# Kernel optimization log

Hardware: AMD Instinct MI355X
Metric: run time of the kernel (lower is better)

## Reference

```python
import jax, jax.numpy as jnp
import numpy as np

N_SAMPLES = 131072
N_FRAMES = 128
CPD = 16
WINDOW = 1024
N_VOICES = 8
N_BLOCKS = 3
N_CP = 512
N_VERBS = 8
MAX_ACTIVE = 32
BASE_RES = 0.5
MAX_GAIN = 5.0
B = 4
E = 16


def fft_convolve(a, b):
    # linear convolution via zero-padded rFFT, truncated to input length
    n = a.shape[-1]
    fa = jnp.fft.rfft(a, n=2 * n, axis=-1)
    fb = jnp.fft.rfft(b, n=2 * n, axis=-1)
    return jnp.fft.irfft(fa * fb, n=2 * n, axis=-1)[..., :n]


def sparsify(x, k):
    # keep top-k entries of the whole control plane, zero the rest
    flat = x.reshape(-1)
    vals, idx = jax.lax.top_k(flat, k)
    return jnp.zeros_like(flat).at[idx].set(vals).reshape(x.shape)


def run_layer(cp, w1, decays, w2, audio_map, gains):
    # cp: [CPD, F]
    frames = cp.shape[-1]
    x = w1 @ cp
    orig = x
    logd = jnp.log(1e-12 + decays)  # [CPD]
    env = jnp.exp(jnp.cumsum(jnp.broadcast_to(logd[:, None], (CPD, frames)), axis=-1))
    x = fft_convolve(x, env)
    x = w2 @ x + orig
    cp_out = jnp.tanh(x * gains[:, None])
    audio = (audio_map @ cp_out).T.reshape(-1)  # [F*WINDOW], frame-major
    return audio, cp_out


def stack_forward(cp, w1s, w2s, audios, decays_p, gains_p, mix):
    wc = cp
    outs = []
    for i in range(N_BLOCKS):
        d = BASE_RES + jax.nn.sigmoid(decays_p[i]) * (1.0 - BASE_RES)
        g = jax.nn.sigmoid(gains_p[i]) * MAX_GAIN
        out, wc = run_layer(jax.nn.relu(wc), w1s[i], d, w2s[i], audios[i], g)
        outs.append(out)
    channels = jnp.stack(outs, axis=0)  # [N_BLOCKS, N_SAMPLES]
    mixed = jnp.einsum('ct,c->t', channels, jax.nn.softmax(mix))
    return mixed / (jnp.max(jnp.abs(mixed)) + 1e-8)  # max_norm


def event_forward(voice_l, cp_choice, amp, room_l, room_mix_l, times,
                  cp_items, verbs, w1, w2, audio_maps, decays, gains, mix):
    vidx = jnp.argmax(voice_l)  # hard voice one-hot (normalize=True -> value 1.0)
    cp = cp_items[jnp.argmax(cp_choice)].reshape(CPD, N_FRAMES)
    cp = sparsify(cp / (cp.sum() + 1e-8), MAX_ACTIVE)
    samples = stack_forward(cp, w1[vidx], w2[vidx], audio_maps[vidx],
                            decays[vidx], gains[vidx], mix[vidx])  # [N_SAMPLES]
    verb = verbs[jnp.argmax(room_l)]  # hard reverb lookup
    wet = fft_convolve(verb, samples)
    vm = jax.nn.softmax(room_mix_l)  # [wet, dry]
    final = wet * vm[0] + samples * vm[1]
    final = final * jnp.abs(amp[0])
    # DiracScheduler: upsample-with-holes then FFT convolve
    step = N_SAMPLES // N_FRAMES
    impulse = jnp.zeros(N_SAMPLES, final.dtype).at[jnp.arange(N_FRAMES) * step].set(times)
    return fft_convolve(final, impulse)


def setup_inputs():
    key = jax.random.key(0)
    ks = jax.random.split(key, 14)
    return {
        'voice': jax.random.normal(ks[0], (B, E, N_VOICES), jnp.float32),
        'control_plane_choice': jax.random.normal(ks[1], (B, E, N_CP), jnp.float32),
        'amplitudes': jax.random.uniform(ks[2], (B, E, 1), jnp.float32),
        'room_choice': jax.random.normal(ks[3], (B, E, N_VERBS), jnp.float32),
        'room_mix': jax.random.normal(ks[4], (B, E, 2), jnp.float32),
        'times': jax.random.uniform(ks[5], (B, E, N_FRAMES), jnp.float32),
        'cp_items': jax.random.uniform(ks[6], (N_CP, N_FRAMES * CPD), jnp.float32),
        'verbs': jax.random.normal(ks[7], (N_VERBS, N_SAMPLES), jnp.float32) * 0.01,
        'w1': jax.random.normal(ks[8], (N_VOICES, N_BLOCKS, CPD, CPD), jnp.float32) * 0.01,
        'w2': jax.random.normal(ks[9], (N_VOICES, N_BLOCKS, CPD, CPD), jnp.float32) * 0.01,
        'audio_maps': jax.random.normal(ks[10], (N_VOICES, N_BLOCKS, WINDOW, CPD), jnp.float32) * 0.01,
        'decays': jax.random.normal(ks[11], (N_VOICES, N_BLOCKS, CPD), jnp.float32),
        'gains': jax.random.normal(ks[12], (N_VOICES, N_BLOCKS, CPD), jnp.float32),
        'mix': jax.random.normal(ks[13], (N_VOICES, N_BLOCKS), jnp.float32),
    }


def reference(voice, control_plane_choice, amplitudes, room_choice, room_mix, times,
              cp_items, verbs, w1, w2, audio_maps, decays, gains, mix):
    per_event = jax.vmap(jax.vmap(event_forward, in_axes=(0,) * 6 + (None,) * 8),
                         in_axes=(0,) * 6 + (None,) * 8)
    return per_event(voice, control_plane_choice, amplitudes, room_choice, room_mix, times,
                     cp_items, verbs, w1, w2, audio_maps, decays, gains, mix)
```

## Files before the change

### kernel.cpp

```cpp
#include <hip/hip_runtime.h>
#include <math.h>

#define NS 131072
#define NFR 128
#define CPDIM 16
#define WIN 1024
#define NVOICE 8
#define NBLK 3
#define NCP 512
#define NVERB 8
#define NEV 64
#define N1 1024
#define NBINS 1025

struct EvParams {
  int vidx, cpidx, ridx;
  float vm0, vm1, amp;
  float mixw0, mixw1, mixw2;
  unsigned int maxslot;
  int pad[6];
};

__global__ void kt_tw(float2* __restrict__ tw) {
  int k = blockIdx.x * 256 + threadIdx.x;
  if (k < 1024) {
    float ang = -3.067961575771282340e-03f * (float)k;
    float s, c;
    sincosf(ang, &s, &c);
    tw[k] = make_float2(c, s);
  }
}

__device__ __forceinline__ void fft1024(float* re, float* im, const float2* twl,
                                        int tid, bool inverse) {
  #pragma unroll
  for (int s = 1; s <= 10; ++s) {
    const int half = 1 << (s - 1);
    const int tsh = 11 - s;
    for (int k = tid; k < 512; k += 256) {
      int j = k & (half - 1);
      int i0 = ((k ^ j) << 1) | j;
      int i1 = i0 + half;
      float2 w = twl[j << tsh];
      float wr = w.x, wi = inverse ? -w.y : w.y;
      float xr = re[i1], xi = im[i1];
      float tr = wr * xr - wi * xi;
      float ti = wr * xi + wi * xr;
      float ur = re[i0], ui = im[i0];
      re[i0] = ur + tr; im[i0] = ui + ti;
      re[i1] = ur - tr; im[i1] = ui - ti;
    }
    __syncthreads();
  }
}

__device__ __forceinline__ void rfft_fwd(const float2* __restrict__ src2, float scale,
                                         float2* __restrict__ dst,
                                         float* re, float* im, float2* twl,
                                         const float2* __restrict__ twg, int tid) {
  for (int i = tid; i < 1024; i += 256) twl[i] = twg[i];
  for (int n = tid; n < 1024; n += 256) {
    int r = __brev(n) >> 22;
    if (n < 512) {
      float2 x = src2[n];
      re[r] = x.x * scale; im[r] = x.y * scale;
    } else { re[r] = 0.0f; im[r] = 0.0f; }
  }
  __syncthreads();
  fft1024(re, im, twl, tid, false);
  for (int k = tid; k <= 1024; k += 256) {
    int km = (1024 - k) & 1023;
    float zr = re[k & 1023], zi = im[k & 1023];
    float mr = re[km], mi = im[km];
    float Are = 0.5f * (zr + mr), Aim = 0.5f * (zi - mi);
    float Bre = 0.5f * (zi + mi), Bim = 0.5f * (mr - zr);
    float wr, wi;
    if (k == 1024) { wr = -1.0f; wi = 0.0f; }
    else { float2 w = twl[k]; wr = w.x; wi = w.y; }
    dst[k] = make_float2(Are + wr * Bre - wi * Bim, Aim + wr * Bim + wi * Bre);
  }
}

__global__ void k0_params(const float* __restrict__ voice, const float* __restrict__ cpc,
                          const float* __restrict__ amps, const float* __restrict__ roomc,
                          const float* __restrict__ roomm, const float* __restrict__ mix,
                          EvParams* __restrict__ P) {
  int e = blockIdx.x;
  int tid = threadIdx.x;
  __shared__ float bvals[64];
  __shared__ int bidx[64];

  if (tid == 0) {
    const float* v = voice + e * NVOICE;
    int vi = 0; float bv = v[0];
    for (int i = 1; i < NVOICE; ++i) if (v[i] > bv) { bv = v[i]; vi = i; }
    P[e].vidx = vi;

    const float* r = roomc + e * NVERB;
    int ri = 0; float br = r[0];
    for (int i = 1; i < NVERB; ++i) if (r[i] > br) { br = r[i]; ri = i; }
    P[e].ridx = ri;

    float m0 = roomm[e * 2 + 0], m1 = roomm[e * 2 + 1];
    float mx = fmaxf(m0, m1);
    float e0 = expf(m0 - mx), e1 = expf(m1 - mx);
    float inv = 1.0f / (e0 + e1);
    P[e].vm0 = e0 * inv;
    P[e].vm1 = e1 * inv;
    P[e].amp = fabsf(amps[e]);

    const float* mm = mix + vi * NBLK;
    float mmx = fmaxf(fmaxf(mm[0], mm[1]), mm[2]);
    float w0 = expf(mm[0] - mmx), w1 = expf(mm[1] - mmx), w2 = expf(mm[2] - mmx);
    float si = 1.0f / (w0 + w1 + w2);
    P[e].mixw0 = w0 * si; P[e].mixw1 = w1 * si; P[e].mixw2 = w2 * si;
    P[e].maxslot = 0u;
  }

  const float* c = cpc + (size_t)e * NCP;
  float bv = -INFINITY; int bi = 0;
  for (int i = tid; i < NCP; i += 64) {
    float x = c[i];
    if (x > bv) { bv = x; bi = i; }
  }
  bvals[tid] = bv; bidx[tid] = bi;
  __syncthreads();
  if (tid == 0) {
    float best = bvals[0]; int besti = bidx[0];
    for (int i = 1; i < 64; ++i) {
      if (bvals[i] > best || (bvals[i] == best && bidx[i] < besti)) { best = bvals[i]; besti = bidx[i]; }
    }
    P[e].cpidx = besti;
  }
}

__global__ __launch_bounds__(256) void kv_fft(const float* __restrict__ verbs,
                                              const float2* __restrict__ twg,
                                              float2* __restrict__ Vhat) {
  __shared__ float re[N1], im[N1];
  __shared__ float2 twl[N1];
  int v = blockIdx.x >> 7, j = blockIdx.x & 127;
  int tid = threadIdx.x;
  rfft_fwd((const float2*)(verbs + (size_t)v * NS + j * WIN), 1.0f,
           Vhat + ((size_t)v * NFR + j) * NBINS, re, im, twl, twg, tid);
}

__global__ __launch_bounds__(256) void k1a_synth(const float* __restrict__ cp_items,
                                                 const float* __restrict__ w1_all,
                                                 const float* __restrict__ w2_all,
                                                 const float* __restrict__ decays,
                                                 const float* __restrict__ gains,
                                                 const EvParams* __restrict__ P,
                                                 float* __restrict__ cp_out_all) {
  __shared__ float cpv[2048];
  __shared__ float wc[2048], xb[2048], yb[2048];
  __shared__ float w1s[256], w2s[256];
  __shared__ float dv[16], gv[16];
  __shared__ float rv[256];
  __shared__ int ri[256];
  __shared__ float s_scale;

  int e = blockIdx.x, tid = threadIdx.x;
  int vidx = P[e].vidx, cpidx = P[e].cpidx;

  float ls = 0.0f;
  for (int i = tid; i < 2048; i += 256) {
    float x = cp_items[(size_t)cpidx * 2048 + i];
    cpv[i] = x;
    ls += x;
  }
  rv[tid] = ls;
  __syncthreads();
  for (int s = 128; s > 0; s >>= 1) { if (tid < s) rv[tid] += rv[tid + s]; __syncthreads(); }
  if (tid == 0) s_scale = 1.0f / (rv[0] + 1e-8f);
  for (int i = tid; i < 2048; i += 256) wc[i] = 0.0f;
  __syncthreads();
  float scale = s_scale;

  for (int it = 0; it < 32; ++it) {
    float bv = -1.0f; int bi = 1 << 30;
    for (int i = tid; i < 2048; i += 256) {
      float x = cpv[i];
      if (x > bv) { bv = x; bi = i; }
    }
    rv[tid] = bv; ri[tid] = bi;
    __syncthreads();
    for (int s = 128; s > 0; s >>= 1) {
      if (tid < s) {
        float ov = rv[tid + s]; int oi = ri[tid + s];
        if (ov > rv[tid] || (ov == rv[tid] && oi < ri[tid])) { rv[tid] = ov; ri[tid] = oi; }
      }
      __syncthreads();
    }
    if (tid == 0) { int mi = ri[0]; wc[mi] = cpv[mi] * scale; cpv[mi] = -2.0f; }
    __syncthreads();
  }

  for (int l = 0; l < NBLK; ++l) {
    int wbase = (vidx * NBLK + l) * 256;
    w1s[tid] = w1_all[wbase + tid];
    w2s[tid] = w2_all[wbase + tid];
    if (tid < 16) {
      float dp = decays[(vidx * NBLK + l) * 16 + tid];
      float sd = 1.0f / (1.0f + expf(-dp));
      dv[tid] = 1e-12f + 0.5f + 0.5f * sd;
      float gp = gains[(vidx * NBLK + l) * 16 + tid];
      gv[tid] = 5.0f / (1.0f + expf(-gp));
    }
    __syncthreads();
    for (int i = tid; i < 2048; i += 256) {
      int cch = i >> 7, f = i & 127;
      float acc = 0.0f;
      #pragma unroll
      for (int k = 0; k < 16; ++k) acc += w1s[cch * 16 + k] * fmaxf(wc[k * 128 + f], 0.0f);
      xb[i] = acc;
    }
    __syncthreads();
    if (tid < 16) {
      float a = 0.0f, d = dv[tid];
      for (int t = 0; t < 128; ++t) { a = d * (a + xb[tid * 128 + t]); yb[tid * 128 + t] = a; }
    }
    __syncthreads();
    for (int i = tid; i < 2048; i += 256) {
      int cch = i >> 7, f = i & 127;
      float acc = xb[i];
      #pragma unroll
      for (int k = 0; k < 16; ++k) acc += w2s[cch * 16 + k] * yb[k * 128 + f];
      float co = tanhf(acc * gv[cch]);
      wc[i] = co;
      cp_out_all[((size_t)e * NBLK + l) * 2048 + i] = co;
    }
    __syncthreads();
  }
}

__global__ __launch_bounds__(256) void k1b_audio(const float* __restrict__ amaps,
                                                 const float* __restrict__ cp_out_all,
                                                 EvParams* __restrict__ P,
                                                 float* __restrict__ mixed) {
  __shared__ float cps[NBLK][16][16];
  __shared__ float red[256];
  int e = blockIdx.x >> 3, fg = blockIdx.x & 7;
  int f0 = fg * 16, tid = threadIdx.x;
  int vidx = P[e].vidx;
  float mw[3] = {P[e].mixw0, P[e].mixw1, P[e].mixw2};

  for (int i = tid; i < NBLK * 256; i += 256) {
    int bl = i >> 8, r = i & 255, cch = r >> 4, fl = r & 15;
    cps[bl][cch][fl] = cp_out_all[((size_t)e * NBLK + bl) * 2048 + cch * 128 + f0 + fl];
  }
  __syncthreads();

  float amax = 0.0f;
  for (int jw = 0; jw < 4; ++jw) {
    int w = jw * 256 + tid;
    float am[NBLK][16];
    #pragma unroll
    for (int bl = 0; bl < NBLK; ++bl) {
      const float* ap = amaps + (((size_t)(vidx * NBLK + bl)) * WIN + w) * CPDIM;
      #pragma unroll
      for (int cch = 0; cch < 16; ++cch) am[bl][cch] = ap[cch] * mw[bl];
    }
    for (int fl = 0; fl < 16; ++fl) {
      float acc = 0.0f;
      #pragma unroll
      for (int bl = 0; bl < NBLK; ++bl)
        #pragma unroll
        for (int cch = 0; cch < 16; ++cch) acc += am[bl][cch] * cps[bl][cch][fl];
      mixed[(size_t)e * NS + (size_t)(f0 + fl) * WIN + w] = acc;
      amax = fmaxf(amax, fabsf(acc));
    }
  }
  red[tid] = amax;
  __syncthreads();
  for (int s = 128; s > 0; s >>= 1) { if (tid < s) red[tid] = fmaxf(red[tid], red[tid + s]); __syncthreads(); }
  if (tid == 0) atomicMax(&P[e].maxslot, __float_as_uint(red[0]));
}

__global__ __launch_bounds__(256) void k2_fwd(const float* __restrict__ mixed,
                                              const EvParams* __restrict__ P,
                                              const float2* __restrict__ twg,
                                              float2* __restrict__ Shat) {
  __shared__ float re[N1], im[N1];
  __shared__ float2 twl[N1];
  int e = blockIdx.x >> 7, p = blockIdx.x & 127;
  int tid = threadIdx.x;
  float invn = 1.0f / (__uint_as_float(P[e].maxslot) + 1e-8f);
  rfft_fwd((const float2*)(mixed + (size_t)e * NS + p * WIN), invn,
           Shat + ((size_t)e * NFR + p) * NBINS, re, im, twl, twg, tid);
}

__global__ __launch_bounds__(256, 4) void k3_conv(const float2* __restrict__ Shat,
                                                  const float2* __restrict__ Vhat,
                                                  const float* __restrict__ times_g,
                                                  const EvParams* __restrict__ P,
                                                  float2* __restrict__ Ohat) {
  __shared__ float Sre[128 * 16], Sim[128 * 16];
  __shared__ float Vre[128 * 16], Vim[128 * 16];
  __shared__ float tms[128];

  int bx = blockIdx.x;
  int e = bx / 65, bg = bx % 65;
  int bin0 = bg * 16;
  int tid = threadIdx.x;
  int b = tid & 15, pg = tid >> 4;
  int p0 = pg * 8;

  int ridx = P[e].ridx;
  float vm0 = P[e].vm0, vm1 = P[e].vm1, amp = P[e].amp;

  const float2* Sg = Shat + (size_t)e * NFR * NBINS;
  const float2* Vg = Vhat + (size_t)ridx * NFR * NBINS;
  for (int i = tid; i < 2048; i += 256) {
    int f = i >> 4, bb = i & 15;
    int bin = bin0 + bb; if (bin > 1024) bin = 1024;
    float2 s = Sg[f * NBINS + bin];
    Sre[i] = s.x; Sim[i] = s.y;
    float2 v = Vg[f * NBINS + bin];
    Vre[i] = v.x; Vim[i] = v.y;
  }
  if (tid < 128) tms[tid] = times_g[e * NFR + tid];
  __syncthreads();

  float ar[8], ai[8];
  #pragma unroll
  for (int t = 0; t < 8; ++t) { ar[t] = 0.0f; ai[t] = 0.0f; }

  for (int ft = 0; ft < pg; ++ft) {
    int f0v = ft * 8;
    float sr[8], si[8];
    #pragma unroll
    for (int ff = 0; ff < 8; ++ff) { int f = f0v + ff; sr[ff] = Sre[f * 16 + b]; si[ff] = Sim[f * 16 + b]; }
    float vr[15], vi[15];
    int jb = p0 - f0v - 7;
    #pragma unroll
    for (int m = 0; m < 15; ++m) { int j = jb + m; vr[m] = Vre[j * 16 + b]; vi[m] = Vim[j * 16 + b]; }
    #pragma unroll
    for (int ff = 0; ff < 8; ++ff) {
      #pragma unroll
      for (int t = 0; t < 8; ++t) {
        int m = 7 - ff + t;
        ar[t] += sr[ff] * vr[m] - si[ff] * vi[m];
        ai[t] += sr[ff] * vi[m] + si[ff] * vr[m];
      }
    }
  }
  {
    float sr[8], si[8];
    #pragma unroll
    for (int ff = 0; ff < 8; ++ff) { int f = p0 + ff; sr[ff] = Sre[f * 16 + b]; si[ff] = Sim[f * 16 + b]; }
    float vr[8], vi[8];
    #pragma unroll
    for (int m = 0; m < 8; ++m) { vr[m] = Vre[m * 16 + b]; vi[m] = Vim[m * 16 + b]; }
    #pragma unroll
    for (int ff = 0; ff < 8; ++ff) {
      #pragma unroll
      for (int t = 0; t < 8; ++t) {
        if (t >= ff) {
          int m = t - ff;
          ar[t] += sr[ff] * vr[m] - si[ff] * vi[m];
          ai[t] += sr[ff] * vi[m] + si[ff] * vr[m];
        }
      }
    }
  }

  __syncthreads();
  #pragma unroll
  for (int t = 0; t < 8; ++t) {
    int p = p0 + t;
    float sre = Sre[p * 16 + b], sim = Sim[p * 16 + b];
    Vre[p * 16 + b] = amp * (vm0 * ar[t] + vm1 * sre);
    Vim[p * 16 + b] = amp * (vm0 * ai[t] + vm1 * sim);
  }
  __syncthreads();

  #pragma unroll
  for (int t = 0; t < 8; ++t) { ar[t] = 0.0f; ai[t] = 0.0f; }

  for (int ft = 0; ft < pg; ++ft) {
    int f0v = ft * 8;
    float trr[8];
    #pragma unroll
    for (int ff = 0; ff < 8; ++ff) trr[ff] = tms[f0v + ff];
    float ur[15], ui[15];
    int jb = p0 - f0v - 7;
    #pragma unroll
    for (int m = 0; m < 15; ++m) { int j = jb + m; ur[m] = Vre[j * 16 + b]; ui[m] = Vim[j * 16 + b]; }
    #pragma unroll
    for (int ff = 0; ff < 8; ++ff) {
      #pragma unroll
      for (int t = 0; t < 8; ++t) {
        int m = 7 - ff + t;
        ar[t] += trr[ff] * ur[m];
        ai[t] += trr[ff] * ui[m];
      }
    }
  }
  {
    float trr[8];
    #pragma unroll
    for (int ff = 0; ff < 8; ++ff) trr[ff] = tms[p0 + ff];
    float ur[8], ui[8];
    #pragma unroll
    for (int m = 0; m < 8; ++m) { ur[m] = Vre[m * 16 + b]; ui[m] = Vim[m * 16 + b]; }
    #pragma unroll
    for (int ff = 0; ff < 8; ++ff) {
      #pragma unroll
      for (int t = 0; t < 8; ++t) {
        if (t >= ff) {
          int m = t - ff;
          ar[t] += trr[ff] * ur[m];
          ai[t] += trr[ff] * ui[m];
        }
      }
    }
  }

  int bin = bin0 + b;
  if (bin <= 1024) {
    float2* Og = Ohat + (size_t)e * NFR * NBINS;
    #pragma unroll
    for (int t = 0; t < 8; ++t) {
      Og[(p0 + t) * NBINS + bin] = make_float2(ar[t], ai[t]);
    }
  }
}

__global__ __launch_bounds__(256) void k4_ifft(const float2* __restrict__ Ohat,
                                               const float2* __restrict__ twg,
                                               float* __restrict__ out,
                                               float* __restrict__ tail) {
  __shared__ float re[N1], im[N1];
  __shared__ float2 twl[N1];
  int e = blockIdx.x >> 7, p = blockIdx.x & 127;
  int tid = threadIdx.x;
  const float2* src = Ohat + ((size_t)e * NFR + p) * NBINS;
  for (int i = tid; i < 1024; i += 256) twl[i] = twg[i];
  __syncthreads();
  for (int k = tid; k < 1024; k += 256) {
    float2 Xk = src[k];
    float2 Xm = src[1024 - k];
    float Are = 0.5f * (Xk.x + Xm.x), Aim = 0.5f * (Xk.y - Xm.y);
    float Dre = 0.5f * (Xk.x - Xm.x), Dim = 0.5f * (Xk.y + Xm.y);
    float2 w = twl[k];
    float Bre = w.x * Dre + w.y * Dim;
    float Bim = w.x * Dim - w.y * Dre;
    int r = __brev(k) >> 22;
    re[r] = Are - Bim;
    im[r] = Aim + Bre;
  }
  __syncthreads();
  fft1024(re, im, twl, tid, true);
  const float inv = 1.0f / (float)N1;
  float2* o2 = (float2*)(out + (size_t)e * NS + (size_t)p * WIN);
  for (int n = tid; n < 512; n += 256) o2[n] = make_float2(re[n] * inv, im[n] * inv);
  float2* t2 = (float2*)(tail + ((size_t)e * NFR + p) * WIN);
  for (int n = tid; n < 512; n += 256) t2[n] = make_float2(re[n + 512] * inv, im[n + 512] * inv);
}

__global__ __launch_bounds__(256) void k5_tail(const float* __restrict__ tail, float* __restrict__ out) {
  size_t idx = (size_t)blockIdx.x * 256 + threadIdx.x;
  if (idx >= (size_t)NEV * 127 * WIN) return;
  int u = (int)(idx & 1023);
  size_t rest = idx >> 10;
  int pm1 = (int)(rest % 127);
  int e = (int)(rest / 127);
  int p = pm1 + 1;
  out[(size_t)e * NS + (size_t)p * WIN + u] += tail[((size_t)e * NFR + pm1) * WIN + u];
}

extern "C" void kernel_launch(void* const* d_in, const int* in_sizes, int n_in,
                              void* d_out, int out_size, void* d_ws, size_t ws_size,
                              hipStream_t stream) {
  (void)in_sizes; (void)n_in; (void)out_size; (void)ws_size;
  const float* voice    = (const float*)d_in[0];
  const float* cpc      = (const float*)d_in[1];
  const float* amps     = (const float*)d_in[2];
  const float* roomc    = (const float*)d_in[3];
  const float* roomm    = (const float*)d_in[4];
  const float* times    = (const float*)d_in[5];
  const float* cp_items = (const float*)d_in[6];
  const float* verbs    = (const float*)d_in[7];
  const float* w1       = (const float*)d_in[8];
  const float* w2       = (const float*)d_in[9];
  const float* amaps    = (const float*)d_in[10];
  const float* decays   = (const float*)d_in[11];
  const float* gains    = (const float*)d_in[12];
  const float* mix      = (const float*)d_in[13];
  float* out = (float*)d_out;

  char* base = (char*)d_ws;
  EvParams* P       = (EvParams*)base;
  float2* twg       = (float2*)(base + 4096);
  float* cp_out_all = (float*)(base + 4096 + 8192);
  float* mixed      = cp_out_all + (size_t)393216;
  float2* Shat      = (float2*)(mixed + (size_t)8388608);
  float2* Vhat      = Shat + (size_t)NEV * NFR * NBINS;
  float* tail  = mixed;
  float2* Ohat = Shat;

  kt_tw<<<4, 256, 0, stream>>>(twg);
  k0_params<<<NEV, 64, 0, stream>>>(voice, cpc, amps, roomc, roomm, mix, P);
  kv_fft<<<NVERB * NFR, 256, 0, stream>>>(verbs, twg, Vhat);
  k1a_synth<<<NEV, 256, 0, stream>>>(cp_items, w1, w2, decays, gains, P, cp_out_all);
  k1b_audio<<<NEV * 8, 256, 0, stream>>>(amaps, cp_out_all, P, mixed);
  k2_fwd<<<NEV * NFR, 256, 0, stream>>>(mixed, P, twg, Shat);
  k3_conv<<<NEV * 65, 256, 0, stream>>>(Shat, Vhat, times, P, Ohat);
  k4_ifft<<<NEV * NFR, 256, 0, stream>>>(Ohat, twg, out, tail);
  k5_tail<<<(NEV * 127 * WIN) / 256, 256, 0, stream>>>(tail, out);
}
```

Baseline: 558.6 us.

## Pad FFT shared arrays, split twiddles, warp-shuffle top-k, atomic overlap-add

Several changes land together. The FFT shared buffers get padding to avoid bank conflicts, and twiddles are split into separate real and imaginary arrays. Spectra use a padded row stride, and k3 stores complex values as float2 with a stride of 17. The top-k sparsify in k1a now keeps values in registers and uses wavefront shuffles instead of shared-memory tree reductions. The separate tail kernel is removed: the output is zeroed first and k4 overlap-adds directly with atomicAdd, which adds an extra full-output zeroing pass and atomic traffic in exchange.

```diff
diff --git a/kernel.cpp b/kernel.cpp
--- a/kernel.cpp
+++ b/kernel.cpp
@@ -12,6 +12,8 @@
 #define NEV 64
 #define N1 1024
 #define NBINS 1025
+#define NBP 1032
+#define IDX(i) ((i) + ((i) >> 5))
 
 struct EvParams {
   int vidx, cpidx, ridx;
@@ -31,7 +33,13 @@
   }
 }
 
-__device__ __forceinline__ void fft1024(float* re, float* im, const float2* twl,
+__global__ __launch_bounds__(256) void kz_zero(float4* __restrict__ out4) {
+  size_t i = (size_t)blockIdx.x * 256 + threadIdx.x;
+  out4[i] = make_float4(0.f, 0.f, 0.f, 0.f);
+}
+
+__device__ __forceinline__ void fft1024(float* re, float* im,
+                                        const float* twr, const float* twi,
                                         int tid, bool inverse) {
   #pragma unroll
   for (int s = 1; s <= 10; ++s) {
@@ -40,9 +48,11 @@
     for (int k = tid; k < 512; k += 256) {
       int j = k & (half - 1);
       int i0 = ((k ^ j) << 1) | j;
-      int i1 = i0 + half;
-      float2 w = twl[j << tsh];
-      float wr = w.x, wi = inverse ? -w.y : w.y;
+      int i1 = IDX(i0 + half);
+      i0 = IDX(i0);
+      float wr = twr[j << tsh];
+      float wi = twi[j << tsh];
+      if (inverse) wi = -wi;
       float xr = re[i1], xi = im[i1];
       float tr = wr * xr - wi * xi;
       float ti = wr * xi + wi * xr;
@@ -56,27 +66,27 @@
 
 __device__ __forceinline__ void rfft_fwd(const float2* __restrict__ src2, float scale,
                                          float2* __restrict__ dst,
-                                         float* re, float* im, float2* twl,
+                                         float* re, float* im, float* twr, float* twi,
                                          const float2* __restrict__ twg, int tid) {
-  for (int i = tid; i < 1024; i += 256) twl[i] = twg[i];
+  for (int i = tid; i < 1024; i += 256) { float2 w = twg[i]; twr[i] = w.x; twi[i] = w.y; }
   for (int n = tid; n < 1024; n += 256) {
-    int r = __brev(n) >> 22;
+    int r = IDX(__brev(n) >> 22);
     if (n < 512) {
       float2 x = src2[n];
       re[r] = x.x * scale; im[r] = x.y * scale;
     } else { re[r] = 0.0f; im[r] = 0.0f; }
   }
   __syncthreads();
-  fft1024(re, im, twl, tid, false);
+  fft1024(re, im, twr, twi, tid, false);
   for (int k = tid; k <= 1024; k += 256) {
     int km = (1024 - k) & 1023;
-    float zr = re[k & 1023], zi = im[k & 1023];
-    float mr = re[km], mi = im[km];
+    float zr = re[IDX(k & 1023)], zi = im[IDX(k & 1023)];
+    float mr = re[IDX(km)], mi = im[IDX(km)];
     float Are = 0.5f * (zr + mr), Aim = 0.5f * (zi - mi);
     float Bre = 0.5f * (zi + mi), Bim = 0.5f * (mr - zr);
     float wr, wi;
     if (k == 1024) { wr = -1.0f; wi = 0.0f; }
-    else { float2 w = twl[k]; wr = w.x; wi = w.y; }
+    else { wr = twr[k]; wi = twi[k]; }
     dst[k] = make_float2(Are + wr * Bre - wi * Bim, Aim + wr * Bim + wi * Bre);
   }
 }
@@ -137,12 +147,12 @@
 __global__ __launch_bounds__(256) void kv_fft(const float* __restrict__ verbs,
                                               const float2* __restrict__ twg,
                                               float2* __restrict__ Vhat) {
-  __shared__ float re[N1], im[N1];
-  __shared__ float2 twl[N1];
+  __shared__ float re[N1 + 32], im[N1 + 32];
+  __shared__ float twr[N1], twi[N1];
   int v = blockIdx.x >> 7, j = blockIdx.x & 127;
   int tid = threadIdx.x;
   rfft_fwd((const float2*)(verbs + (size_t)v * NS + j * WIN), 1.0f,
-           Vhat + ((size_t)v * NFR + j) * NBINS, re, im, twl, twg, tid);
+           Vhat + ((size_t)v * NFR + j) * NBP, re, im, twr, twi, twg, tid);
 }
 
 __global__ __launch_bounds__(256) void k1a_synth(const float* __restrict__ cp_items,
@@ -152,47 +162,52 @@
                                                  const float* __restrict__ gains,
                                                  const EvParams* __restrict__ P,
                                                  float* __restrict__ cp_out_all) {
-  __shared__ float cpv[2048];
   __shared__ float wc[2048], xb[2048], yb[2048];
   __shared__ float w1s[256], w2s[256];
   __shared__ float dv[16], gv[16];
-  __shared__ float rv[256];
-  __shared__ int ri[256];
+  __shared__ float rv[4];
+  __shared__ int ri[4];
   __shared__ float s_scale;
 
   int e = blockIdx.x, tid = threadIdx.x;
   int vidx = P[e].vidx, cpidx = P[e].cpidx;
-
+  int base = tid * 8;
+
+  float vals[8];
   float ls = 0.0f;
-  for (int i = tid; i < 2048; i += 256) {
-    float x = cp_items[(size_t)cpidx * 2048 + i];
-    cpv[i] = x;
-    ls += x;
-  }
-  rv[tid] = ls;
-  __syncthreads();
-  for (int s = 128; s > 0; s >>= 1) { if (tid < s) rv[tid] += rv[tid + s]; __syncthreads(); }
-  if (tid == 0) s_scale = 1.0f / (rv[0] + 1e-8f);
+  #pragma unroll
+  for (int q = 0; q < 8; ++q) {
+    float x = cp_items[(size_t)cpidx * 2048 + base + q];
+    vals[q] = x; ls += x;
+  }
+  #pragma unroll
+  for (int off = 32; off > 0; off >>= 1) ls += __shfl_xor(ls, off);
+  if ((tid & 63) == 0) rv[tid >> 6] = ls;
+  __syncthreads();
+  if (tid == 0) s_scale = 1.0f / (rv[0] + rv[1] + rv[2] + rv[3] + 1e-8f);
   for (int i = tid; i < 2048; i += 256) wc[i] = 0.0f;
   __syncthreads();
   float scale = s_scale;
 
   for (int it = 0; it < 32; ++it) {
     float bv = -1.0f; int bi = 1 << 30;
-    for (int i = tid; i < 2048; i += 256) {
-      float x = cpv[i];
-      if (x > bv) { bv = x; bi = i; }
-    }
-    rv[tid] = bv; ri[tid] = bi;
-    __syncthreads();
-    for (int s = 128; s > 0; s >>= 1) {
-      if (tid < s) {
-        float ov = rv[tid + s]; int oi = ri[tid + s];
-        if (ov > rv[tid] || (ov == rv[tid] && oi < ri[tid])) { rv[tid] = ov; ri[tid] = oi; }
-      }
-      __syncthreads();
-    }
-    if (tid == 0) { int mi = ri[0]; wc[mi] = cpv[mi] * scale; cpv[mi] = -2.0f; }
+    #pragma unroll
+    for (int q = 0; q < 8; ++q) {
+      if (vals[q] > bv) { bv = vals[q]; bi = base + q; }
+    }
+    #pragma unroll
+    for (int off = 32; off > 0; off >>= 1) {
+      float ov = __shfl_xor(bv, off); int oi = __shfl_xor(bi, off);
+      if (ov > bv || (ov == bv && oi < bi)) { bv = ov; bi = oi; }
+    }
+    if ((tid & 63) == 0) { rv[tid >> 6] = bv; ri[tid >> 6] = bi; }
+    __syncthreads();
+    float wv = rv[0]; int wi = ri[0];
+    #pragma unroll
+    for (int w = 1; w < 4; ++w) {
+      if (rv[w] > wv || (rv[w] == wv && ri[w] < wi)) { wv = rv[w]; wi = ri[w]; }
+    }
+    if ((wi >> 3) == tid) { vals[wi & 7] = -2.0f; wc[wi] = wv * scale; }
     __syncthreads();
   }
 
@@ -281,13 +296,13 @@
                                               const EvParams* __restrict__ P,
                                               const float2* __restrict__ twg,
                                               float2* __restrict__ Shat) {
-  __shared__ float re[N1], im[N1];
-  __shared__ float2 twl[N1];
+  __shared__ float re[N1 + 32], im[N1 + 32];
+  __shared__ float twr[N1], twi[N1];
   int e = blockIdx.x >> 7, p = blockIdx.x & 127;
   int tid = threadIdx.x;
   float invn = 1.0f / (__uint_as_float(P[e].maxslot) + 1e-8f);
   rfft_fwd((const float2*)(mixed + (size_t)e * NS + p * WIN), invn,
-           Shat + ((size_t)e * NFR + p) * NBINS, re, im, twl, twg, tid);
+           Shat + ((size_t)e * NFR + p) * NBP, re, im, twr, twi, twg, tid);
 }
 
 __global__ __launch_bounds__(256, 4) void k3_conv(const float2* __restrict__ Shat,
@@ -295,8 +310,8 @@
                                                   const float* __restrict__ times_g,
                                                   const EvParams* __restrict__ P,
                                                   float2* __restrict__ Ohat) {
-  __shared__ float Sre[128 * 16], Sim[128 * 16];
-  __shared__ float Vre[128 * 16], Vim[128 * 16];
+  __shared__ float2 S2[128 * 17];
+  __shared__ float2 V2[128 * 17];
   __shared__ float tms[128];
 
   int bx = blockIdx.x;
@@ -309,15 +324,13 @@
   int ridx = P[e].ridx;
   float vm0 = P[e].vm0, vm1 = P[e].vm1, amp = P[e].amp;
 
-  const float2* Sg = Shat + (size_t)e * NFR * NBINS;
-  const float2* Vg = Vhat + (size_t)ridx * NFR * NBINS;
+  const float2* Sg = Shat + (size_t)e * NFR * NBP;
+  const float2* Vg = Vhat + (size_t)ridx * NFR * NBP;
   for (int i = tid; i < 2048; i += 256) {
     int f = i >> 4, bb = i & 15;
     int bin = bin0 + bb; if (bin > 1024) bin = 1024;
-    float2 s = Sg[f * NBINS + bin];
-    Sre[i] = s.x; Sim[i] = s.y;
-    float2 v = Vg[f * NBINS + bin];
-    Vre[i] = v.x; Vim[i] = v.y;
+    S2[f * 17 + bb] = Sg[f * NBP + bin];
+    V2[f * 17 + bb] = Vg[f * NBP + bin];
   }
   if (tid < 128) tms[tid] = times_g[e * NFR + tid];
   __syncthreads();
@@ -328,38 +341,38 @@
 
   for (int ft = 0; ft < pg; ++ft) {
     int f0v = ft * 8;
-    float sr[8], si[8];
-    #pragma unroll
-    for (int ff = 0; ff < 8; ++ff) { int f = f0v + ff; sr[ff] = Sre[f * 16 + b]; si[ff] = Sim[f * 16 + b]; }
-    float vr[15], vi[15];
+    float2 s[8];
+    #pragma unroll
+    for (int ff = 0; ff < 8; ++ff) s[ff] = S2[(f0v + ff) * 17 + b];
+    float2 v[15];
     int jb = p0 - f0v - 7;
     #pragma unroll
-    for (int m = 0; m < 15; ++m) { int j = jb + m; vr[m] = Vre[j * 16 + b]; vi[m] = Vim[j * 16 + b]; }
+    for (int m = 0; m < 15; ++m) v[m] = V2[(jb + m) * 17 + b];
     #pragma unroll
     for (int ff = 0; ff < 8; ++ff) {
       #pragma unroll
       for (int t = 0; t < 8; ++t) {
         int m = 7 - ff + t;
-        ar[t] += sr[ff] * vr[m] - si[ff] * vi[m];
-        ai[t] += sr[ff] * vi[m] + si[ff] * vr[m];
+        ar[t] += s[ff].x * v[m].x - s[ff].y * v[m].y;
+        ai[t] += s[ff].x * v[m].y + s[ff].y * v[m].x;
       }
     }
   }
   {
-    float sr[8], si[8];
-    #pragma unroll
-    for (int ff = 0; ff < 8; ++ff) { int f = p0 + ff; sr[ff] = Sre[f * 16 + b]; si[ff] = Sim[f * 16 + b]; }
-    float vr[8], vi[8];
-    #pragma unroll
-    for (int m = 0; m < 8; ++m) { vr[m] = Vre[m * 16 + b]; vi[m] = Vim[m * 16 + b]; }
+    float2 s[8];
+    #pragma unroll
+    for (int ff = 0; ff < 8; ++ff) s[ff] = S2[(p0 + ff) * 17 + b];
+    float2 v[8];
+    #pragma unroll
+    for (int m = 0; m < 8; ++m) v[m] = V2[m * 17 + b];
     #pragma unroll
     for (int ff = 0; ff < 8; ++ff) {
       #pragma unroll
       for (int t = 0; t < 8; ++t) {
         if (t >= ff) {
           int m = t - ff;
-          ar[t] += sr[ff] * vr[m] - si[ff] * vi[m];
-          ai[t] += sr[ff] * vi[m] + si[ff] * vr[m];
+          ar[t] += s[ff].x * v[m].x - s[ff].y * v[m].y;
+          ai[t] += s[ff].x * v[m].y + s[ff].y * v[m].x;
         }
       }
     }
@@ -369,9 +382,9 @@
   #pragma unroll
   for (int t = 0; t < 8; ++t) {
     int p = p0 + t;
-    float sre = Sre[p * 16 + b], sim = Sim[p * 16 + b];
-    Vre[p * 16 + b] = amp * (vm0 * ar[t] + vm1 * sre);
-    Vim[p * 16 + b] = amp * (vm0 * ai[t] + vm1 * sim);
+    float2 sv = S2[p * 17 + b];
+    V2[p * 17 + b] = make_float2(amp * (vm0 * ar[t] + vm1 * sv.x),
+                                 amp * (vm0 * ai[t] + vm1 * sv.y));
   }
   __syncthreads();
 
@@ -383,17 +396,17 @@
     float trr[8];
     #pragma unroll
     for (int ff = 0; ff < 8; ++ff) trr[ff] = tms[f0v + ff];
-    float ur[15], ui[15];
+    float2 u[15];
     int jb = p0 - f0v - 7;
     #pragma unroll
-    for (int m = 0; m < 15; ++m) { int j = jb + m; ur[m] = Vre[j * 16 + b]; ui[m] = Vim[j * 16 + b]; }
+    for (int m = 0; m < 15; ++m) u[m] = V2[(jb + m) * 17 + b];
     #pragma unroll
     for (int ff = 0; ff < 8; ++ff) {
       #pragma unroll
       for (int t = 0; t < 8; ++t) {
         int m = 7 - ff + t;
-        ar[t] += trr[ff] * ur[m];
-        ai[t] += trr[ff] * ui[m];
+        ar[t] += trr[ff] * u[m].x;
+        ai[t] += trr[ff] * u[m].y;
       }
     }
   }
@@ -401,17 +414,17 @@
     float trr[8];
     #pragma unroll
     for (int ff = 0; ff < 8; ++ff) trr[ff] = tms[p0 + ff];
-    float ur[8], ui[8];
-    #pragma unroll
-    for (int m = 0; m < 8; ++m) { ur[m] = Vre[m * 16 + b]; ui[m] = Vim[m * 16 + b]; }
+    float2 u[8];
+    #pragma unroll
+    for (int m = 0; m < 8; ++m) u[m] = V2[m * 17 + b];
     #pragma unroll
     for (int ff = 0; ff < 8; ++ff) {
       #pragma unroll
       for (int t = 0; t < 8; ++t) {
         if (t >= ff) {
           int m = t - ff;
-          ar[t] += trr[ff] * ur[m];
-          ai[t] += trr[ff] * ui[m];
+          ar[t] += trr[ff] * u[m].x;
+          ai[t] += trr[ff] * u[m].y;
         }
       }
     }
@@ -419,55 +432,45 @@
 
   int bin = bin0 + b;
   if (bin <= 1024) {
-    float2* Og = Ohat + (size_t)e * NFR * NBINS;
+    float2* Og = Ohat + (size_t)e * NFR * NBP;
     #pragma unroll
     for (int t = 0; t < 8; ++t) {
-      Og[(p0 + t) * NBINS + bin] = make_float2(ar[t], ai[t]);
+      Og[(p0 + t) * NBP + bin] = make_float2(ar[t], ai[t]);
     }
   }
 }
 
 __global__ __launch_bounds__(256) void k4_ifft(const float2* __restrict__ Ohat,
                                                const float2* __restrict__ twg,
-                                               float* __restrict__ out,
-                                               float* __restrict__ tail) {
-  __shared__ float re[N1], im[N1];
-  __shared__ float2 twl[N1];
+                                               float* __restrict__ out) {
+  __shared__ float re[N1 + 32], im[N1 + 32];
+  __shared__ float twr[N1], twi[N1];
   int e = blockIdx.x >> 7, p = blockIdx.x & 127;
   int tid = threadIdx.x;
-  const float2* src = Ohat + ((size_t)e * NFR + p) * NBINS;
-  for (int i = tid; i < 1024; i += 256) twl[i] = twg[i];
+  const float2* src = Ohat + ((size_t)e * NFR + p) * NBP;
+  for (int i = tid; i < 1024; i += 256) { float2 w = twg[i]; twr[i] = w.x; twi[i] = w.y; }
   __syncthreads();
   for (int k = tid; k < 1024; k += 256) {
     float2 Xk = src[k];
     float2 Xm = src[1024 - k];
     float Are = 0.5f * (Xk.x + Xm.x), Aim = 0.5f * (Xk.y - Xm.y);
     float Dre = 0.5f * (Xk.x - Xm.x), Dim = 0.5f * (Xk.y + Xm.y);
-    float2 w = twl[k];
-    float Bre = w.x * Dre + w.y * Dim;
-    float Bim = w.x * Dim - w.y * Dre;
-    int r = __brev(k) >> 22;
+    float wr = twr[k], wi = twi[k];
+    float Bre = wr * Dre + wi * Dim;
+    float Bim = wr * Dim - wi * Dre;
+    int r = IDX(__brev(k) >> 22);
     re[r] = Are - Bim;
     im[r] = Aim + Bre;
   }
   __syncthreads();
-  fft1024(re, im, twl, tid, true);
+  fft1024(re, im, twr, twi, tid, true);
   const float inv = 1.0f / (float)N1;
-  float2* o2 = (float2*)(out + (size_t)e * NS + (size_t)p * WIN);
-  for (int n = tid; n < 512; n += 256) o2[n] = make_float2(re[n] * inv, im[n] * inv);
-  float2* t2 = (float2*)(tail + ((size_t)e * NFR + p) * WIN);
-  for (int n = tid; n < 512; n += 256) t2[n] = make_float2(re[n + 512] * inv, im[n + 512] * inv);
-}
-
-__global__ __launch_bounds__(256) void k5_tail(const float* __restrict__ tail, float* __restrict__ out) {
-  size_t idx = (size_t)blockIdx.x * 256 + threadIdx.x;
-  if (idx >= (size_t)NEV * 127 * WIN) return;
-  int u = (int)(idx & 1023);
-  size_t rest = idx >> 10;
-  int pm1 = (int)(rest % 127);
-  int e = (int)(rest / 127);
-  int p = pm1 + 1;
-  out[(size_t)e * NS + (size_t)p * WIN + u] += tail[((size_t)e * NFR + pm1) * WIN + u];
+  float* o = out + (size_t)e * NS + (size_t)p * WIN;
+  int nmax = (p == 127) ? 512 : 1024;
+  for (int n = tid; n < nmax; n += 256) {
+    atomicAdd(&o[2 * n],     re[IDX(n)] * inv);
+    atomicAdd(&o[2 * n + 1], im[IDX(n)] * inv);
+  }
 }
 
 extern "C" void kernel_launch(void* const* d_in, const int* in_sizes, int n_in,
@@ -496,17 +499,16 @@
   float* cp_out_all = (float*)(base + 4096 + 8192);
   float* mixed      = cp_out_all + (size_t)393216;
   float2* Shat      = (float2*)(mixed + (size_t)8388608);
-  float2* Vhat      = Shat + (size_t)NEV * NFR * NBINS;
-  float* tail  = mixed;
+  float2* Vhat      = Shat + (size_t)NEV * NFR * NBP;
   float2* Ohat = Shat;
 
   kt_tw<<<4, 256, 0, stream>>>(twg);
+  kz_zero<<<(NEV * NS / 4) / 256, 256, 0, stream>>>((float4*)out);
   k0_params<<<NEV, 64, 0, stream>>>(voice, cpc, amps, roomc, roomm, mix, P);
   kv_fft<<<NVERB * NFR, 256, 0, stream>>>(verbs, twg, Vhat);
   k1a_synth<<<NEV, 256, 0, stream>>>(cp_items, w1, w2, decays, gains, P, cp_out_all);
   k1b_audio<<<NEV * 8, 256, 0, stream>>>(amaps, cp_out_all, P, mixed);
   k2_fwd<<<NEV * NFR, 256, 0, stream>>>(mixed, P, twg, Shat);
   k3_conv<<<NEV * 65, 256, 0, stream>>>(Shat, Vhat, times, P, Ohat);
-  k4_ifft<<<NEV * NFR, 256, 0, stream>>>(Ohat, twg, out, tail);
-  k5_tail<<<(NEV * 127 * WIN) / 256, 256, 0, stream>>>(tail, out);
-}
+  k4_ifft<<<NEV * NFR, 256, 0, stream>>>(Ohat, twg, out);
+}
```

After: 732.6 us. 1.31x slower.
